# Kernel optimization log

Measured on AMD Instinct MI355X. Metric: run time of the kernel, lower is better.

Reference implementation:

```python
import jax, jax.numpy as jnp
import numpy as np

B, S, D = 4, 4096, 512
HEADS, NS, NEXT = 8, 32, 2048
HD = D // HEADS
SCALE = 1.0 / np.sqrt(HD)


def setup_inputs() -> dict:
    key = jax.random.key(0)
    ks = jax.random.split(key, 12)
    w_scale = 1.0 / np.sqrt(D)
    return {
        "sequence_tokens": jax.random.normal(ks[0], (B, S, D), jnp.float32),
        "sequence_mask": jnp.ones((B, S), dtype=bool),
        "ns_tokens": jax.random.normal(ks[1], (B, NS, D), jnp.float32),
        "ns_mask": jnp.ones((B, NS), dtype=bool),
        "next_sequence_length": NEXT,
        "Wq": jax.random.normal(ks[2], (D, D), jnp.float32) * w_scale,
        "Wk": jax.random.normal(ks[3], (D, D), jnp.float32) * w_scale,
        "Wv": jax.random.normal(ks[4], (D, D), jnp.float32) * w_scale,
        "ns_q_w": jax.random.normal(ks[5], (NS, D, D), jnp.float32) * w_scale,
        "ns_k_w": jax.random.normal(ks[6], (NS, D, D), jnp.float32) * w_scale,
        "ns_v_w": jax.random.normal(ks[7], (NS, D, D), jnp.float32) * w_scale,
        "Wo": jax.random.normal(ks[8], (D, D), jnp.float32) * w_scale,
    }


def reference(sequence_tokens, sequence_mask, ns_tokens, ns_mask,
              next_sequence_length, Wq, Wk, Wv, ns_q_w, ns_k_w, ns_v_w, Wo):
    b, s, d = sequence_tokens.shape
    ns = ns_tokens.shape[1]
    nxt = next_sequence_length

    seq_q = sequence_tokens[:, -nxt:]
    seq_q_mask = sequence_mask[:, -nxt:]

    # mixed projections: standard linear for seq tokens, per-position weights for NS tokens
    q = jnp.concatenate([seq_q @ Wq.T,
                         jnp.einsum('bnd,ndo->bno', ns_tokens, ns_q_w)], axis=1)
    k = jnp.concatenate([sequence_tokens @ Wk.T,
                         jnp.einsum('bnd,ndo->bno', ns_tokens, ns_k_w)], axis=1)
    v = jnp.concatenate([sequence_tokens @ Wv.T,
                         jnp.einsum('bnd,ndo->bno', ns_tokens, ns_v_w)], axis=1)

    def heads(x):  # [b, t, d] -> [b, h, t, hd]
        return x.reshape(b, -1, HEADS, HD).transpose(0, 2, 1, 3)
    q, k, v = heads(q), heads(k), heads(v)

    total = s + ns
    q_pos = jnp.concatenate([jnp.arange(s - nxt, s), jnp.arange(s, total)])
    k_pos = jnp.arange(total)
    causal = k_pos[None, :] <= q_pos[:, None]              # [Q, K]
    key_mask = jnp.concatenate([sequence_mask, ns_mask], axis=1)  # [b, K]

    logits = jnp.einsum('bhqd,bhkd->bhqk',
                        q.astype(jnp.float32), k.astype(jnp.float32)) * SCALE
    logits = jnp.where(causal[None, None], logits, -10000.0)
    logits = jnp.where(key_mask[:, None, None, :], logits, -10000.0)
    w = jax.nn.softmax(logits, axis=-1).astype(q.dtype)

    att = jnp.einsum('bhqk,bhkd->bhqd', w, v)
    att = att.transpose(0, 2, 1, 3).reshape(b, nxt + ns, d)
    att = att @ Wo.T

    seq_out = att[:, :nxt] * seq_q_mask[..., None].astype(att.dtype)
    ns_out = att[:, nxt:] * ns_mask[..., None].astype(att.dtype)
    return (seq_out, ns_out)
```

## Files before the change

kernel.cpp:

```cpp
#include <hip/hip_runtime.h>

#define NBATCH 4
#define SEQ    4096
#define DMODEL 512
#define NHEAD  8
#define HDIM   64
#define NSN    32
#define NXT    2048
#define QLEN   2080
#define KLEN   4128

using bf16x8 = __attribute__((ext_vector_type(8))) short;
using f32x4  = __attribute__((ext_vector_type(4))) float;

typedef __attribute__((address_space(1))) unsigned int gu32;
typedef __attribute__((address_space(3))) unsigned int lu32;

#define QSCALE 0.18033688f

__device__ __forceinline__ unsigned short f2bf(float f) {
  unsigned int u = __float_as_uint(f);
  u += 0x7FFF + ((u >> 16) & 1);
  return (unsigned short)(u >> 16);
}

__device__ __forceinline__ float bf2f(unsigned short u) {
  return __uint_as_float((unsigned int)u << 16);
}

__device__ __forceinline__ f32x4 mfma16(bf16x8 a, bf16x8 b, f32x4 c) {
  return __builtin_amdgcn_mfma_f32_16x16x32_bf16(a, b, c, 0, 0, 0);
}

__device__ __forceinline__ void gload_lds16(const void* g, void* lds_base) {
  __builtin_amdgcn_global_load_lds((const gu32*)g, (lu32*)lds_base, 16, 0, 0);
}

__device__ __forceinline__ unsigned int cvt_pk_bf16(float lo, float hi) {
  unsigned int r;
  asm("v_cvt_pk_bf16_f32 %0, %1, %2" : "=v"(r) : "v"(lo), "v"(hi));
  return r;
}

__global__ __launch_bounds__(256) void cvt_f32_bf16_v4(const float* __restrict__ src,
                                                       unsigned short* __restrict__ dst, int n4) {
  int i = blockIdx.x * 256 + threadIdx.x;
  if (i >= n4) return;
  float4 v = reinterpret_cast<const float4*>(src)[i];
  ushort4 r;
  r.x = f2bf(v.x); r.y = f2bf(v.y); r.z = f2bf(v.z); r.w = f2bf(v.w);
  reinterpret_cast<ushort4*>(dst)[i] = r;
}

__global__ __launch_bounds__(256) void cvt_w4(const float* __restrict__ a, const float* __restrict__ b,
                                              const float* __restrict__ c, const float* __restrict__ d,
                                              unsigned short* __restrict__ dst) {
  const float* s = blockIdx.y == 0 ? a : blockIdx.y == 1 ? b : blockIdx.y == 2 ? c : d;
  int i = blockIdx.x * 256 + threadIdx.x;
  float4 v = reinterpret_cast<const float4*>(s)[i];
  ushort4 r;
  r.x = f2bf(v.x); r.y = f2bf(v.y); r.z = f2bf(v.z); r.w = f2bf(v.w);
  reinterpret_cast<ushort4*>(dst)[(size_t)blockIdx.y * 65536 + i] = r;
}

__global__ __launch_bounds__(256) void proj_gemm(const unsigned short* __restrict__ X,
                                                 const unsigned short* __restrict__ W,
                                                 unsigned short* __restrict__ Out,
                                                 int rpb_shift, int row_off, int out_L, float scale) {
  __shared__ unsigned short As[128 * 32];
  __shared__ unsigned short Bs[128 * 32];
  const int tid = threadIdx.x;
  const int w = tid >> 6, l = tid & 63;
  const int lg = l >> 4, lr = l & 15;
  const int row0 = blockIdx.x * 128, col0 = blockIdx.y * 128;
  const int wr = (w >> 1) * 64, wc = (w & 1) * 64;
  const int mask = (1 << rpb_shift) - 1;

  f32x4 acc[4][4];
#pragma unroll
  for (int m = 0; m < 4; ++m)
#pragma unroll
    for (int n = 0; n < 4; ++n) acc[m][n] = (f32x4){0.f, 0.f, 0.f, 0.f};

  const int sr = w * 16 + (l >> 2);
  const int sc = (l & 3) * 8;

  for (int k0 = 0; k0 < 512; k0 += 32) {
#pragma unroll
    for (int i = 0; i < 2; ++i) {
      int gr = row0 + sr + i * 64;
      int xrow = ((gr >> rpb_shift) << 12) + row_off + (gr & mask);
      const unsigned short* gpa = X + (size_t)xrow * 512 + k0 + sc;
      gload_lds16(gpa, (char*)As + i * 4096 + w * 1024);
      const unsigned short* gpb = W + (size_t)(col0 + sr + i * 64) * 512 + k0 + sc;
      gload_lds16(gpb, (char*)Bs + i * 4096 + w * 1024);
    }
    __syncthreads();
    bf16x8 av[4], bv[4];
#pragma unroll
    for (int m = 0; m < 4; ++m) av[m] = *(const bf16x8*)&As[(wr + m * 16 + lr) * 32 + lg * 8];
#pragma unroll
    for (int n = 0; n < 4; ++n) bv[n] = *(const bf16x8*)&Bs[(wc + n * 16 + lr) * 32 + lg * 8];
#pragma unroll
    for (int m = 0; m < 4; ++m)
#pragma unroll
      for (int n = 0; n < 4; ++n) acc[m][n] = mfma16(av[m], bv[n], acc[m][n]);
    __syncthreads();
  }

#pragma unroll
  for (int m = 0; m < 4; ++m) {
    int crow = row0 + wr + m * 16 + lg * 4;
#pragma unroll
    for (int n = 0; n < 4; ++n) {
      int ccol = col0 + wc + n * 16 + lr;
      int hh = ccol >> 6, dd = ccol & 63;
#pragma unroll
      for (int r = 0; r < 4; ++r) {
        int cr = crow + r;
        int bb = cr >> rpb_shift, ii = cr & mask;
        Out[(((size_t)bb * NHEAD + hh) * out_L + ii) * HDIM + dd] = f2bf(acc[m][n][r] * scale);
      }
    }
  }
}

__global__ __launch_bounds__(256) void ns_proj(const float* __restrict__ nst,
                                               const float* __restrict__ Wnq, const float* __restrict__ Wnk,
                                               const float* __restrict__ Wnv,
                                               unsigned short* __restrict__ Qb, unsigned short* __restrict__ Kb,
                                               unsigned short* __restrict__ Vb) {
  const int oc = blockIdx.x, n = blockIdx.y, p = blockIdx.z;
  const float* W = p == 0 ? Wnq : p == 1 ? Wnk : Wnv;
  unsigned short* Out = p == 0 ? Qb : p == 1 ? Kb : Vb;
  const int out_L = p == 0 ? QLEN : KLEN;
  const int orow = p == 0 ? NXT + n : SEQ + n;
  const float scale = p == 0 ? QSCALE : 1.f;

  __shared__ float xs[NBATCH][DMODEL];
  __shared__ float red[NBATCH][128];
  const int tid = threadIdx.x;
  for (int idx = tid; idx < NBATCH * DMODEL; idx += 256)
    xs[idx >> 9][idx & 511] = nst[(size_t)((idx >> 9) * NSN + n) * DMODEL + (idx & 511)];
  __syncthreads();

  const int o = oc * 128 + (tid & 127);
  const int dh = tid >> 7;
  float a0 = 0.f, a1 = 0.f, a2 = 0.f, a3 = 0.f;
  const float* wp = W + (size_t)n * DMODEL * DMODEL + o;
#pragma unroll 8
  for (int d = dh * 256; d < dh * 256 + 256; ++d) {
    float wv = wp[(size_t)d * DMODEL];
    a0 += xs[0][d] * wv; a1 += xs[1][d] * wv; a2 += xs[2][d] * wv; a3 += xs[3][d] * wv;
  }
  if (dh == 1) { red[0][tid & 127] = a0; red[1][tid & 127] = a1; red[2][tid & 127] = a2; red[3][tid & 127] = a3; }
  __syncthreads();
  if (dh == 0) {
    a0 += red[0][tid & 127]; a1 += red[1][tid & 127]; a2 += red[2][tid & 127]; a3 += red[3][tid & 127];
    int hh = o >> 6, dd = o & 63;
    float v[4] = {a0, a1, a2, a3};
#pragma unroll
    for (int b = 0; b < NBATCH; ++b)
      Out[(((size_t)b * NHEAD + hh) * out_L + orow) * HDIM + dd] = f2bf(v[b] * scale);
  }
}

__global__ __launch_bounds__(256) void vtrans(const unsigned short* __restrict__ V,
                                              unsigned short* __restrict__ Vt) {
  __shared__ unsigned short t[64 * 64];
  const int tid = threadIdx.x;
  const int kv0 = blockIdx.x * 64, bh = blockIdx.y;
  const unsigned short* Vhp = V + (size_t)bh * KLEN * HDIM;
  unsigned short* Vtp = Vt + (size_t)bh * HDIM * KLEN;

#pragma unroll
  for (int i = 0; i < 2; ++i) {
    int c = i * 256 + tid;
    int row = c >> 3, c8 = c & 7;
    int kvg = kv0 + row; if (kvg > KLEN - 1) kvg = KLEN - 1;
    int4 v4 = *(const int4*)(Vhp + (size_t)kvg * HDIM + c8 * 8);
    *(int4*)&t[row * 64 + ((c8 ^ ((row >> 3) & 7)) * 8)] = v4;
  }
  __syncthreads();
#pragma unroll
  for (int i = 0; i < 2; ++i) {
    int c = i * 256 + tid;
    int d = c >> 3, k8 = c & 7;
    if (kv0 + k8 * 8 <= KLEN - 8) {
      unsigned int wd[4];
#pragma unroll
      for (int jj = 0; jj < 4; ++jj) {
        int ka = k8 * 8 + jj * 2, kb2 = ka + 1;
        unsigned int lo = t[ka  * 64 + (((d >> 3) ^ ((ka  >> 3) & 7)) * 8) + (d & 7)];
        unsigned int hi = t[kb2 * 64 + (((d >> 3) ^ ((kb2 >> 3) & 7)) * 8) + (d & 7)];
        wd[jj] = lo | (hi << 16);
      }
      int4 o; o.x = wd[0]; o.y = wd[1]; o.z = wd[2]; o.w = wd[3];
      *(int4*)(Vtp + (size_t)d * KLEN + kv0 + k8 * 8) = o;
    }
  }
}

__global__ __launch_bounds__(256) void attn_kernel(const unsigned short* __restrict__ Qb,
                                                   const unsigned short* __restrict__ Kb,
                                                   const unsigned short* __restrict__ Vtg,
                                                   unsigned short* __restrict__ PoA,
                                                   float2* __restrict__ PmlA,
                                                   unsigned short* __restrict__ PoB,
                                                   float2* __restrict__ PmlB) {
  __shared__ unsigned short Ks[64 * 64];
  __shared__ unsigned short Vs[64 * 64];

  const int tid = threadIdx.x;
  const int w = tid >> 6, l = tid & 63;
  const int lg = l >> 4, lr = l & 15;
  const bool geven = (l & 16) == 0;
  const int bx = (int)blockIdx.x;
  const int qb = 32 - bx / 3;
  const int sp = bx - 3 * (32 - qb);
  const int bh = (int)blockIdx.z * NHEAD + (int)blockIdx.y;
  const int q0 = qb * 64;
  const int base = NXT + q0;
  const int nkb = (base >> 6) + 1;
  const int t0 = (sp * nkb) / 3;
  const int t1 = ((sp + 1) * nkb) / 3;

  const unsigned short* Qh = Qb + (size_t)bh * QLEN * HDIM;
  const unsigned short* Kh = Kb + (size_t)bh * KLEN * HDIM;
  const unsigned short* Vh = Vtg + (size_t)bh * HDIM * KLEN;

  int qrow = q0 + w * 16 + lr; if (qrow > QLEN - 1) qrow = QLEN - 1;
  const bf16x8 qa0 = *(const bf16x8*)(Qh + (size_t)qrow * HDIM + lg * 8);
  const bf16x8 qa1 = *(const bf16x8*)(Qh + (size_t)qrow * HDIM + 32 + lg * 8);

  f32x4 acc[4];
#pragma unroll
  for (int n = 0; n < 4; ++n) acc[n] = (f32x4){0.f, 0.f, 0.f, 0.f};
  float m_r = 0.f, lsum = 0.f;

  const bf16x8 ones = {(short)0x3F80, (short)0x3F80, (short)0x3F80, (short)0x3F80,
                       (short)0x3F80, (short)0x3F80, (short)0x3F80, (short)0x3F80};

  const int rloc = l >> 3;
  const int jsrc = ((l & 7) ^ rloc) * 8;

  for (int kb = t0; kb < t1; ++kb) {
    const int kv0 = kb * 64;
    if (kv0 + 64 <= KLEN) {
#pragma unroll
      for (int i = 0; i < 2; ++i) {
        const int r8 = (w * 2 + i) * 8;
        gload_lds16(Kh + (size_t)(kv0 + r8 + rloc) * HDIM + jsrc, &Ks[r8 * 64]);
        gload_lds16(Vh + (size_t)(r8 + rloc) * KLEN + kv0 + jsrc, &Vs[r8 * 64]);
      }
    } else {
#pragma unroll
      for (int i = 0; i < 2; ++i) {
        const int r8 = (w * 2 + i) * 8;
        int kr = kv0 + r8 + rloc; if (kr > KLEN - 1) kr = KLEN - 1;
        gload_lds16(Kh + (size_t)kr * HDIM + jsrc, &Ks[r8 * 64]);
        int vc = kv0 + jsrc; if (vc > KLEN - 8) vc = KLEN - 8;
        gload_lds16(Vh + (size_t)(r8 + rloc) * KLEN + vc, &Vs[r8 * 64]);
      }
    }
    __syncthreads();

    const f32x4 minit = {-m_r, -m_r, -m_r, -m_r};
    f32x4 s[4];
#pragma unroll
    for (int n = 0; n < 4; ++n) {
      const int rk = n * 16 + lr;
      const bf16x8 k0 = *(const bf16x8*)&Ks[rk * 64 + ((lg ^ (rk & 7)) * 8)];
      const bf16x8 k1 = *(const bf16x8*)&Ks[rk * 64 + (((4 + lg) ^ (rk & 7)) * 8)];
      s[n] = mfma16(k0, qa0, minit);
      s[n] = mfma16(k1, qa1, s[n]);
    }

    if (kb == nkb - 1) {
      const int qk_lim = base + w * 16 + lr;
#pragma unroll
      for (int n = 0; n < 4; ++n)
#pragma unroll
        for (int r = 0; r < 4; ++r)
          if (kv0 + n * 16 + lg * 4 + r > qk_lim) s[n][r] = -1e30f;
    }

    float a3 = fmaxf(fmaxf(s[0][0], s[0][1]), s[0][2]);
    float b3 = fmaxf(fmaxf(s[0][3], s[1][0]), s[1][1]);
    float c3 = fmaxf(fmaxf(s[1][2], s[1][3]), s[2][0]);
    float d3 = fmaxf(fmaxf(s[2][1], s[2][2]), s[2][3]);
    float e3 = fmaxf(fmaxf(s[3][0], s[3][1]), s[3][2]);
    float rl = fmaxf(fmaxf(a3, b3), c3);
    rl = fmaxf(fmaxf(rl, d3), e3);
    rl = fmaxf(rl, s[3][3]);

    if (__any(rl > 11.5f)) {
      float rmax = fmaxf(rl, __shfl_xor(rl, 16));
      rmax = fmaxf(rmax, __shfl_xor(rmax, 32));
      float dl = fmaxf(rmax, 0.f);
      float sc = exp2f(-dl);
      lsum *= sc; m_r += dl;
#pragma unroll
      for (int n = 0; n < 4; ++n) {
        acc[n][0] *= sc; acc[n][1] *= sc; acc[n][2] *= sc; acc[n][3] *= sc;
#pragma unroll
        for (int r = 0; r < 4; ++r) s[n][r] = exp2f(s[n][r] - dl);
      }
    } else {
#pragma unroll
      for (int n = 0; n < 4; ++n)
#pragma unroll
        for (int r = 0; r < 4; ++r) s[n][r] = exp2f(s[n][r]);
    }

    unsigned int wpk[4][2];
#pragma unroll
    for (int n = 0; n < 4; ++n) {
      wpk[n][0] = cvt_pk_bf16(s[n][0], s[n][1]);
      wpk[n][1] = cvt_pk_bf16(s[n][2], s[n][3]);
    }
    bf16x8 pb[2];
#pragma unroll
    for (int ks = 0; ks < 2; ++ks) {
      unsigned int A0 = wpk[2 * ks][0], B0 = wpk[2 * ks + 1][0];
      unsigned int A1 = wpk[2 * ks][1], B1 = wpk[2 * ks + 1][1];
      asm("v_permlane32_swap_b32 %0, %1" : "+v"(A0), "+v"(B0));
      asm("v_permlane32_swap_b32 %0, %1" : "+v"(A1), "+v"(B1));
      unsigned int sA0 = __builtin_amdgcn_ds_swizzle(A0, 0x401F);
      unsigned int sA1 = __builtin_amdgcn_ds_swizzle(A1, 0x401F);
      unsigned int sB0 = __builtin_amdgcn_ds_swizzle(B0, 0x401F);
      unsigned int sB1 = __builtin_amdgcn_ds_swizzle(B1, 0x401F);
      int4 words;
      words.x = geven ? A0 : sB0;
      words.y = geven ? A1 : sB1;
      words.z = geven ? sA0 : B0;
      words.w = geven ? sA1 : B1;
      pb[ks] = *(bf16x8*)&words;
    }

    f32x4 acc_s = (f32x4){0.f, 0.f, 0.f, 0.f};
    acc_s = mfma16(ones, pb[0], acc_s);
    acc_s = mfma16(ones, pb[1], acc_s);
    lsum += acc_s[0];

#pragma unroll
    for (int n = 0; n < 4; ++n) {
      const int rv = n * 16 + lr;
#pragma unroll
      for (int ks = 0; ks < 2; ++ks) {
        const bf16x8 vv = *(const bf16x8*)&Vs[rv * 64 + (((ks * 4 + lg) ^ (rv & 7)) * 8)];
        acc[n] = mfma16(vv, pb[ks], acc[n]);
      }
    }

    __syncthreads();
  }

  const int qi = q0 + w * 16 + lr;
  if (qi < QLEN) {
    unsigned short* po; float2* pml; size_t rowp;
    if (sp < 2) { rowp = (size_t)(sp * 32 + bh) * QLEN + qi; po = PoA + rowp * 64; pml = PmlA + rowp; }
    else        { rowp = (size_t)bh * QLEN + qi;             po = PoB + rowp * 64; pml = PmlB + rowp; }
#pragma unroll
    for (int n = 0; n < 4; ++n) {
      ushort4 pk;
      pk.x = f2bf(acc[n][0]); pk.y = f2bf(acc[n][1]);
      pk.z = f2bf(acc[n][2]); pk.w = f2bf(acc[n][3]);
      *(ushort4*)(po + n * 16 + lg * 4) = pk;
    }
    if (l < 16) *pml = (float2){m_r, lsum};
  }
}

__global__ __launch_bounds__(256) void attn_combine(const unsigned short* __restrict__ PoA,
                                                    const float2* __restrict__ PmlA,
                                                    const unsigned short* __restrict__ PoB,
                                                    const float2* __restrict__ PmlB,
                                                    unsigned short* __restrict__ Att) {
  const int bh = blockIdx.y;
  const int idx = blockIdx.x * 256 + threadIdx.x;
  const int qi = idx >> 3, dc = (idx & 7) * 8;
  const size_t row = (size_t)bh * QLEN + qi;
  const float2 ml0 = PmlA[row];
  const float2 ml1 = PmlA[(size_t)32 * QLEN + row];
  const float2 ml2 = PmlB[row];
  const float mm = fmaxf(fmaxf(ml0.x, ml1.x), ml2.x);
  float s0 = exp2f(ml0.x - mm), s1 = exp2f(ml1.x - mm), s2 = exp2f(ml2.x - mm);
  const float inv = 1.f / (ml0.y * s0 + ml1.y * s1 + ml2.y * s2);
  s0 *= inv; s1 *= inv; s2 *= inv;
  const bf16x8 o0 = *(const bf16x8*)(PoA + row * 64 + dc);
  const bf16x8 o1 = *(const bf16x8*)(PoA + ((size_t)32 * QLEN + row) * 64 + dc);
  const bf16x8 o2 = *(const bf16x8*)(PoB + row * 64 + dc);
  unsigned short out[8];
#pragma unroll
  for (int j = 0; j < 8; ++j)
    out[j] = f2bf(bf2f((unsigned short)o0[j]) * s0 + bf2f((unsigned short)o1[j]) * s1 +
                  bf2f((unsigned short)o2[j]) * s2);
  const int b = bh >> 3, h = bh & 7;
  *(int4*)(Att + ((size_t)b * QLEN + qi) * DMODEL + h * HDIM + dc) = *(int4*)out;
}

__global__ __launch_bounds__(256) void out_gemm(const unsigned short* __restrict__ A,
                                                const unsigned short* __restrict__ W,
                                                float* __restrict__ Out) {
  __shared__ unsigned short As[128 * 32];
  __shared__ unsigned short Bs[128 * 32];
  const int tid = threadIdx.x;
  const int w = tid >> 6, l = tid & 63;
  const int lg = l >> 4, lr = l & 15;
  const int row0 = blockIdx.x * 128, col0 = blockIdx.y * 128;
  const int wr = (w >> 1) * 64, wc = (w & 1) * 64;

  f32x4 acc[4][4];
#pragma unroll
  for (int m = 0; m < 4; ++m)
#pragma unroll
    for (int n = 0; n < 4; ++n) acc[m][n] = (f32x4){0.f, 0.f, 0.f, 0.f};

  const int sr = w * 16 + (l >> 2);
  const int sc = (l & 3) * 8;

  for (int k0 = 0; k0 < 512; k0 += 32) {
#pragma unroll
    for (int i = 0; i < 2; ++i) {
      const unsigned short* gpa = A + (size_t)(row0 + sr + i * 64) * 512 + k0 + sc;
      gload_lds16(gpa, (char*)As + i * 4096 + w * 1024);
      const unsigned short* gpb = W + (size_t)(col0 + sr + i * 64) * 512 + k0 + sc;
      gload_lds16(gpb, (char*)Bs + i * 4096 + w * 1024);
    }
    __syncthreads();
    bf16x8 av[4], bv[4];
#pragma unroll
    for (int m = 0; m < 4; ++m) av[m] = *(const bf16x8*)&As[(wr + m * 16 + lr) * 32 + lg * 8];
#pragma unroll
    for (int n = 0; n < 4; ++n) bv[n] = *(const bf16x8*)&Bs[(wc + n * 16 + lr) * 32 + lg * 8];
#pragma unroll
    for (int m = 0; m < 4; ++m)
#pragma unroll
      for (int n = 0; n < 4; ++n) acc[m][n] = mfma16(av[m], bv[n], acc[m][n]);
    __syncthreads();
  }

#pragma unroll
  for (int m = 0; m < 4; ++m) {
    int crow = row0 + wr + m * 16 + lg * 4;
#pragma unroll
    for (int n = 0; n < 4; ++n) {
      int ccol = col0 + wc + n * 16 + lr;
#pragma unroll
      for (int r = 0; r < 4; ++r) {
        int cr = crow + r;
        int bb = cr / QLEN, ii = cr - bb * QLEN;
        size_t off = ii < NXT
                       ? ((size_t)bb * NXT + ii) * DMODEL + ccol
                       : (size_t)NBATCH * NXT * DMODEL + ((size_t)bb * NSN + (ii - NXT)) * DMODEL + ccol;
        Out[off] = acc[m][n][r];
      }
    }
  }
}

extern "C" void kernel_launch(void* const* d_in, const int* in_sizes, int n_in,
                              void* d_out, int out_size, void* d_ws, size_t ws_size,
                              hipStream_t stream) {
  const float* seq = (const float*)d_in[0];
  const float* nst = (const float*)d_in[2];
  const float* Wq  = (const float*)d_in[5];
  const float* Wk  = (const float*)d_in[6];
  const float* Wv  = (const float*)d_in[7];
  const float* nsq = (const float*)d_in[8];
  const float* nsk = (const float*)d_in[9];
  const float* nsv = (const float*)d_in[10];
  const float* Wo  = (const float*)d_in[11];
  float* out = (float*)d_out;

  char* ws = (char*)d_ws;
  unsigned short* Xbf  = (unsigned short*)(ws);
  unsigned short* Wqb  = (unsigned short*)(ws + 16777216);
  unsigned short* Wkb  = Wqb + 262144;
  unsigned short* Wvb  = Wkb + 262144;
  unsigned short* Wob  = Wvb + 262144;
  unsigned short* Qbuf = (unsigned short*)(ws + 18874368);
  unsigned short* Kbuf = (unsigned short*)(ws + 27394048);
  unsigned short* Vbuf = (unsigned short*)(ws + 44302336);
  unsigned short* Att  = (unsigned short*)(ws + 61210624);
  unsigned short* Vtg  = (unsigned short*)(ws + 69730304);
  unsigned short* PoA  = (unsigned short*)(ws);
  float2*         PmlA = (float2*)(ws + 17039360);
  unsigned short* PoB  = (unsigned short*)(ws + 44302336);
  float2*         PmlB = (float2*)(ws + 52822016);
  if (ws_size < 86638592) return;

  cvt_f32_bf16_v4<<<dim3(8192), dim3(256), 0, stream>>>(seq, Xbf, 2097152);
  cvt_w4<<<dim3(256, 4), dim3(256), 0, stream>>>(Wq, Wk, Wv, Wo, Wqb);
  proj_gemm<<<dim3(128, 4), dim3(256), 0, stream>>>(Xbf, Wkb, Kbuf, 12, 0, KLEN, 1.f);
  proj_gemm<<<dim3(128, 4), dim3(256), 0, stream>>>(Xbf, Wvb, Vbuf, 12, 0, KLEN, 1.f);
  proj_gemm<<<dim3(64, 4), dim3(256), 0, stream>>>(Xbf, Wqb, Qbuf, 11, 2048, QLEN, QSCALE);
  ns_proj<<<dim3(4, 32, 3), dim3(256), 0, stream>>>(nst, nsq, nsk, nsv, Qbuf, Kbuf, Vbuf);
  vtrans<<<dim3(65, 32), dim3(256), 0, stream>>>(Vbuf, Vtg);
  attn_kernel<<<dim3(99, 8, 4), dim3(256), 0, stream>>>(Qbuf, Kbuf, Vtg, PoA, PmlA, PoB, PmlB);
  attn_combine<<<dim3(65, 32), dim3(256), 0, stream>>>(PoA, PmlA, PoB, PmlB, Att);
  out_gemm<<<dim3(65, 4), dim3(256), 0, stream>>>(Att, Wob, out);
}
```

Measured before the change: 227.1 us.

## Fuse K/V projection GEMMs, hoist attention load pointers, shrink out_gemm tiles

```diff
diff --git a/kernel.cpp b/kernel.cpp
--- a/kernel.cpp
+++ b/kernel.cpp
@@ -120,6 +120,82 @@
         int cr = crow + r;
         int bb = cr >> rpb_shift, ii = cr & mask;
         Out[(((size_t)bb * NHEAD + hh) * out_L + ii) * HDIM + dd] = f2bf(acc[m][n][r] * scale);
+      }
+    }
+  }
+}
+
+__global__ __launch_bounds__(256)
+__attribute__((amdgpu_waves_per_eu(1, 2)))
+void proj_gemm_kv(const unsigned short* __restrict__ X,
+                  const unsigned short* __restrict__ Wk,
+                  const unsigned short* __restrict__ Wv,
+                  unsigned short* __restrict__ OutK,
+                  unsigned short* __restrict__ OutV) {
+  __shared__ unsigned short As[128 * 32];
+  __shared__ unsigned short Bk[128 * 32];
+  __shared__ unsigned short Bv[128 * 32];
+  const int tid = threadIdx.x;
+  const int w = tid >> 6, l = tid & 63;
+  const int lg = l >> 4, lr = l & 15;
+  const int row0 = blockIdx.x * 128, col0 = blockIdx.y * 128;
+  const int wr = (w >> 1) * 64, wc = (w & 1) * 64;
+
+  f32x4 ak[4][4], av4[4][4];
+#pragma unroll
+  for (int m = 0; m < 4; ++m)
+#pragma unroll
+    for (int n = 0; n < 4; ++n) {
+      ak[m][n] = (f32x4){0.f, 0.f, 0.f, 0.f};
+      av4[m][n] = (f32x4){0.f, 0.f, 0.f, 0.f};
+    }
+
+  const int sr = w * 16 + (l >> 2);
+  const int sc = (l & 3) * 8;
+
+  for (int k0 = 0; k0 < 512; k0 += 32) {
+#pragma unroll
+    for (int i = 0; i < 2; ++i) {
+      const unsigned short* gpa = X + (size_t)(row0 + sr + i * 64) * 512 + k0 + sc;
+      gload_lds16(gpa, (char*)As + i * 4096 + w * 1024);
+      const unsigned short* gpk = Wk + (size_t)(col0 + sr + i * 64) * 512 + k0 + sc;
+      gload_lds16(gpk, (char*)Bk + i * 4096 + w * 1024);
+      const unsigned short* gpv = Wv + (size_t)(col0 + sr + i * 64) * 512 + k0 + sc;
+      gload_lds16(gpv, (char*)Bv + i * 4096 + w * 1024);
+    }
+    __syncthreads();
+    bf16x8 xa[4], bb[4];
+#pragma unroll
+    for (int m = 0; m < 4; ++m) xa[m] = *(const bf16x8*)&As[(wr + m * 16 + lr) * 32 + lg * 8];
+#pragma unroll
+    for (int n = 0; n < 4; ++n) bb[n] = *(const bf16x8*)&Bk[(wc + n * 16 + lr) * 32 + lg * 8];
+#pragma unroll
+    for (int m = 0; m < 4; ++m)
+#pragma unroll
+      for (int n = 0; n < 4; ++n) ak[m][n] = mfma16(xa[m], bb[n], ak[m][n]);
+#pragma unroll
+    for (int n = 0; n < 4; ++n) bb[n] = *(const bf16x8*)&Bv[(wc + n * 16 + lr) * 32 + lg * 8];
+#pragma unroll
+    for (int m = 0; m < 4; ++m)
+#pragma unroll
+      for (int n = 0; n < 4; ++n) av4[m][n] = mfma16(xa[m], bb[n], av4[m][n]);
+    __syncthreads();
+  }
+
+#pragma unroll
+  for (int m = 0; m < 4; ++m) {
+    int crow = row0 + wr + m * 16 + lg * 4;
+#pragma unroll
+    for (int n = 0; n < 4; ++n) {
+      int ccol = col0 + wc + n * 16 + lr;
+      int hh = ccol >> 6, dd = ccol & 63;
+#pragma unroll
+      for (int r = 0; r < 4; ++r) {
+        int cr = crow + r;
+        int bb2 = cr >> 12, ii = cr & 4095;
+        size_t off = (((size_t)bb2 * NHEAD + hh) * KLEN + ii) * HDIM + dd;
+        OutK[off] = f2bf(ak[m][n][r]);
+        OutV[off] = f2bf(av4[m][n][r]);
       }
     }
   }
@@ -243,23 +319,27 @@
 
   const int rloc = l >> 3;
   const int jsrc = ((l & 7) ^ rloc) * 8;
+  const int r8K0 = (w * 2) * 8, r8K1 = (w * 2 + 1) * 8;
+  const unsigned short* kP0 = Kh + (size_t)(t0 * 64 + r8K0 + rloc) * HDIM + jsrc;
+  const unsigned short* kP1 = Kh + (size_t)(t0 * 64 + r8K1 + rloc) * HDIM + jsrc;
+  const unsigned short* vP0 = Vh + (size_t)(r8K0 + rloc) * KLEN + t0 * 64 + jsrc;
+  const unsigned short* vP1 = Vh + (size_t)(r8K1 + rloc) * KLEN + t0 * 64 + jsrc;
 
   for (int kb = t0; kb < t1; ++kb) {
     const int kv0 = kb * 64;
-    if (kv0 + 64 <= KLEN) {
+    if (kb != 64) {
+      gload_lds16(kP0, &Ks[r8K0 * 64]);
+      gload_lds16(kP1, &Ks[r8K1 * 64]);
+      gload_lds16(vP0, &Vs[r8K0 * 64]);
+      gload_lds16(vP1, &Vs[r8K1 * 64]);
+      kP0 += 64 * HDIM; kP1 += 64 * HDIM; vP0 += 64; vP1 += 64;
+    } else {
 #pragma unroll
       for (int i = 0; i < 2; ++i) {
         const int r8 = (w * 2 + i) * 8;
-        gload_lds16(Kh + (size_t)(kv0 + r8 + rloc) * HDIM + jsrc, &Ks[r8 * 64]);
-        gload_lds16(Vh + (size_t)(r8 + rloc) * KLEN + kv0 + jsrc, &Vs[r8 * 64]);
-      }
-    } else {
-#pragma unroll
-      for (int i = 0; i < 2; ++i) {
-        const int r8 = (w * 2 + i) * 8;
-        int kr = kv0 + r8 + rloc; if (kr > KLEN - 1) kr = KLEN - 1;
+        int kr = 4096 + r8 + rloc; if (kr > KLEN - 1) kr = KLEN - 1;
         gload_lds16(Kh + (size_t)kr * HDIM + jsrc, &Ks[r8 * 64]);
-        int vc = kv0 + jsrc; if (vc > KLEN - 8) vc = KLEN - 8;
+        int vc = 4096 + jsrc; if (vc > KLEN - 8) vc = KLEN - 8;
         gload_lds16(Vh + (size_t)(r8 + rloc) * KLEN + vc, &Vs[r8 * 64]);
       }
     }
@@ -403,59 +483,52 @@
 __global__ __launch_bounds__(256) void out_gemm(const unsigned short* __restrict__ A,
                                                 const unsigned short* __restrict__ W,
                                                 float* __restrict__ Out) {
-  __shared__ unsigned short As[128 * 32];
+  __shared__ unsigned short As[64 * 32];
   __shared__ unsigned short Bs[128 * 32];
   const int tid = threadIdx.x;
   const int w = tid >> 6, l = tid & 63;
   const int lg = l >> 4, lr = l & 15;
-  const int row0 = blockIdx.x * 128, col0 = blockIdx.y * 128;
-  const int wr = (w >> 1) * 64, wc = (w & 1) * 64;
-
-  f32x4 acc[4][4];
-#pragma unroll
-  for (int m = 0; m < 4; ++m)
-#pragma unroll
-    for (int n = 0; n < 4; ++n) acc[m][n] = (f32x4){0.f, 0.f, 0.f, 0.f};
-
-  const int sr = w * 16 + (l >> 2);
-  const int sc = (l & 3) * 8;
+  const int row0 = blockIdx.x * 64, col0 = blockIdx.y * 128;
+
+  f32x4 acc[8];
+#pragma unroll
+  for (int n = 0; n < 8; ++n) acc[n] = (f32x4){0.f, 0.f, 0.f, 0.f};
+
+  const int sra = tid >> 2;
+  const int sca = (tid & 3) * 8;
+  const int srb = w * 16 + (l >> 2);
+  const int scb = (l & 3) * 8;
 
   for (int k0 = 0; k0 < 512; k0 += 32) {
+    const unsigned short* gpa = A + (size_t)(row0 + sra) * 512 + k0 + sca;
+    gload_lds16(gpa, (char*)As + w * 1024);
 #pragma unroll
     for (int i = 0; i < 2; ++i) {
-      const unsigned short* gpa = A + (size_t)(row0 + sr + i * 64) * 512 + k0 + sc;
-      gload_lds16(gpa, (char*)As + i * 4096 + w * 1024);
-      const unsigned short* gpb = W + (size_t)(col0 + sr + i * 64) * 512 + k0 + sc;
+      const unsigned short* gpb = W + (size_t)(col0 + srb + i * 64) * 512 + k0 + scb;
       gload_lds16(gpb, (char*)Bs + i * 4096 + w * 1024);
     }
     __syncthreads();
-    bf16x8 av[4], bv[4];
-#pragma unroll
-    for (int m = 0; m < 4; ++m) av[m] = *(const bf16x8*)&As[(wr + m * 16 + lr) * 32 + lg * 8];
-#pragma unroll
-    for (int n = 0; n < 4; ++n) bv[n] = *(const bf16x8*)&Bs[(wc + n * 16 + lr) * 32 + lg * 8];
-#pragma unroll
-    for (int m = 0; m < 4; ++m)
-#pragma unroll
-      for (int n = 0; n < 4; ++n) acc[m][n] = mfma16(av[m], bv[n], acc[m][n]);
-    __syncthreads();
-  }
-
-#pragma unroll
-  for (int m = 0; m < 4; ++m) {
-    int crow = row0 + wr + m * 16 + lg * 4;
-#pragma unroll
-    for (int n = 0; n < 4; ++n) {
-      int ccol = col0 + wc + n * 16 + lr;
-#pragma unroll
-      for (int r = 0; r < 4; ++r) {
-        int cr = crow + r;
-        int bb = cr / QLEN, ii = cr - bb * QLEN;
-        size_t off = ii < NXT
-                       ? ((size_t)bb * NXT + ii) * DMODEL + ccol
-                       : (size_t)NBATCH * NXT * DMODEL + ((size_t)bb * NSN + (ii - NXT)) * DMODEL + ccol;
-        Out[off] = acc[m][n][r];
-      }
+    const bf16x8 avf = *(const bf16x8*)&As[(w * 16 + lr) * 32 + lg * 8];
+#pragma unroll
+    for (int n = 0; n < 8; ++n) {
+      const bf16x8 bv = *(const bf16x8*)&Bs[(n * 16 + lr) * 32 + lg * 8];
+      acc[n] = mfma16(avf, bv, acc[n]);
+    }
+    __syncthreads();
+  }
+
+  const int crow = row0 + w * 16 + lg * 4;
+#pragma unroll
+  for (int n = 0; n < 8; ++n) {
+    const int ccol = col0 + n * 16 + lr;
+#pragma unroll
+    for (int r = 0; r < 4; ++r) {
+      int cr = crow + r;
+      int bb = cr / QLEN, ii = cr - bb * QLEN;
+      size_t off = ii < NXT
+                     ? ((size_t)bb * NXT + ii) * DMODEL + ccol
+                     : (size_t)NBATCH * NXT * DMODEL + ((size_t)bb * NSN + (ii - NXT)) * DMODEL + ccol;
+      Out[off] = acc[n][r];
     }
   }
 }
@@ -493,12 +566,11 @@
 
   cvt_f32_bf16_v4<<<dim3(8192), dim3(256), 0, stream>>>(seq, Xbf, 2097152);
   cvt_w4<<<dim3(256, 4), dim3(256), 0, stream>>>(Wq, Wk, Wv, Wo, Wqb);
-  proj_gemm<<<dim3(128, 4), dim3(256), 0, stream>>>(Xbf, Wkb, Kbuf, 12, 0, KLEN, 1.f);
-  proj_gemm<<<dim3(128, 4), dim3(256), 0, stream>>>(Xbf, Wvb, Vbuf, 12, 0, KLEN, 1.f);
+  proj_gemm_kv<<<dim3(128, 4), dim3(256), 0, stream>>>(Xbf, Wkb, Wvb, Kbuf, Vbuf);
   proj_gemm<<<dim3(64, 4), dim3(256), 0, stream>>>(Xbf, Wqb, Qbuf, 11, 2048, QLEN, QSCALE);
   ns_proj<<<dim3(4, 32, 3), dim3(256), 0, stream>>>(nst, nsq, nsk, nsv, Qbuf, Kbuf, Vbuf);
   vtrans<<<dim3(65, 32), dim3(256), 0, stream>>>(Vbuf, Vtg);
   attn_kernel<<<dim3(99, 8, 4), dim3(256), 0, stream>>>(Qbuf, Kbuf, Vtg, PoA, PmlA, PoB, PmlB);
   attn_combine<<<dim3(65, 32), dim3(256), 0, stream>>>(PoA, PmlA, PoB, PmlB, Att);
-  out_gemm<<<dim3(65, 4), dim3(256), 0, stream>>>(Att, Wob, out);
-}
+  out_gemm<<<dim3(130, 4), dim3(256), 0, stream>>>(Att, Wob, out);
+}
```

New measurement: 241.9 us. 1.06x slower.
